# Performance work log

Measured on AMD Instinct MI355X. Metric: run time of the kernel, lower is better.

The kernel has to match this reference:

```python
import jax, jax.numpy as jnp
import numpy as np

B, C, D, H, W = 2, 64, 8, 32, 32  # identity f/g mappings => intermediate_channels == input_channels == 64


def setup_inputs() -> dict:
    key = jax.random.key(0)
    k1, k2 = jax.random.split(key)
    x = jax.random.normal(k1, (B, C, D, H, W), dtype=jnp.float32)
    # w_mapping: 1x1 conv, intermediate_channels -> input_channels (here 64 -> 64)
    w_weight = jax.random.normal(k2, (C, C), dtype=jnp.float32) * (1.0 / np.sqrt(C))
    w_bias = jnp.zeros((C,), dtype=jnp.float32)
    return {"x": x, "w_weight": w_weight, "w_bias": w_bias}


def reference(x, w_weight, w_bias):
    b, c = x.shape[0], x.shape[1]
    spatial = x.shape[2:]
    n = int(np.prod(spatial))
    # f/g mappings are identity -> q, k, v are all the flattened input
    x_flat = x.reshape(b, c, n)              # [B, C, N]
    q = jnp.transpose(x_flat, (0, 2, 1))     # [B, N, C] (f_mapping_i, permuted)
    k = x_flat                               # [B, C, N] (f_mapping_j)
    v = jnp.transpose(x_flat, (0, 2, 1))     # [B, N, C] (g_x, permuted)
    f = jnp.einsum('bic,bcj->bij', q, k)     # [B, N, N] dot-product similarity
    f_norm = jax.nn.softmax(f, axis=-1)
    y = jnp.einsum('bij,bjc->bic', f_norm, v)  # [B, N, C]
    y = jnp.transpose(y, (0, 2, 1)).reshape(b, c, *spatial)  # [B, C, D, H, W]
    # w_mapping: 1x1 conv (pointwise linear over channels) + bias
    w_y = jnp.einsum('bc...,oc->bo...', y, w_weight) + w_bias.reshape((1, c) + (1,) * len(spatial))
    z = w_y + x  # residual
    return z
```

## Files before the change

### kernel.cpp

```cpp
#include <hip/hip_runtime.h>
#include <hip/hip_bf16.h>


constexpr int NC = 64;
constexpr int NN = 8192;
constexpr int NKV = 128;

typedef __attribute__((ext_vector_type(8))) short bf16x8;
typedef __attribute__((ext_vector_type(4))) float f32x4;

static __device__ __forceinline__ short f2bf(float f) {
    union { float f; unsigned u; } v; v.f = f;
    unsigned r = v.u + 0x7FFFu + ((v.u >> 16) & 1u);
    return (short)(r >> 16);
}
static __device__ __forceinline__ float bf2f(short h) {
    union { unsigned u; float f; } v;
    v.u = ((unsigned)(unsigned short)h) << 16;
    return v.f;
}

__global__ __launch_bounds__(256) void prep_kernel(
    const float* __restrict__ x, short* __restrict__ Xjc, short* __restrict__ Xcj)
{
    __shared__ short T[64 * 64];
    const int tid = threadIdx.x;
    const int jt = blockIdx.x;
    const int b  = blockIdx.y;
    const int bo = b * NC * NN;
    const int sc = tid >> 2, sq = tid & 3;

    const float* xr = x + bo + sc * NN + jt * 64 + sq * 16;
    float fl[16];
    *(float4*)&fl[0]  = *(const float4*)(xr + 0);
    *(float4*)&fl[4]  = *(const float4*)(xr + 4);
    *(float4*)&fl[8]  = *(const float4*)(xr + 8);
    *(float4*)&fl[12] = *(const float4*)(xr + 12);
    short h[16];
    #pragma unroll
    for (int e = 0; e < 16; ++e) h[e] = f2bf(fl[e]);

    bf16x8 v0, v1;
    #pragma unroll
    for (int e = 0; e < 8; ++e) { v0[e] = h[e]; v1[e] = h[8 + e]; }
    *(bf16x8*)&Xcj[bo + sc * NN + jt * 64 + sq * 16]     = v0;
    *(bf16x8*)&Xcj[bo + sc * NN + jt * 64 + sq * 16 + 8] = v1;

    #pragma unroll
    for (int jj = 0; jj < 16; ++jj) {
        int j = sq * 16 + jj;
        T[(j * 64 + sc) ^ ((j & 7) << 3)] = h[jj];
    }
    __syncthreads();

    const int jr = tid >> 2, cq = tid & 3;
    bf16x8 a0 = *(const bf16x8*)&T[(jr * 64 + cq * 16) ^ ((jr & 7) << 3)];
    bf16x8 a1 = *(const bf16x8*)&T[(jr * 64 + cq * 16 + 8) ^ ((jr & 7) << 3)];
    *(bf16x8*)&Xjc[bo + (jt * 64 + jr) * 64 + cq * 16]     = a0;
    *(bf16x8*)&Xjc[bo + (jt * 64 + jr) * 64 + cq * 16 + 8] = a1;
}

__global__ __launch_bounds__(256) void attn_fd_kernel(
    const short* __restrict__ Xjc, const short* __restrict__ Xcj,
    float* __restrict__ ypart, float* __restrict__ lpart, int tps)
{
    __shared__ short Pl[4][32 * 64];

    const int tid  = threadIdx.x;
    const int lane = tid & 63;
    const int wv   = tid >> 6;
    const int lo   = lane & 15;
    const int hi   = lane >> 4;

    const int b  = blockIdx.y;
    const int sp = blockIdx.z;
    const int bo = b * NC * NN;
    const int qbase = blockIdx.x * 128 + wv * 32;
    short* Pw = Pl[wv];

    bf16x8 qf[2][2];
    #pragma unroll
    for (int qs = 0; qs < 2; ++qs)
        #pragma unroll
        for (int kk = 0; kk < 2; ++kk)
            qf[qs][kk] = *(const bf16x8*)&Xjc[bo + (qbase + qs * 16 + lo) * 64 + kk * 32 + hi * 8];

    float mrow[2][4];
    #pragma unroll
    for (int qs = 0; qs < 2; ++qs) {
        float v = 0.0f;
        #pragma unroll
        for (int kk = 0; kk < 2; ++kk)
            #pragma unroll
            for (int e = 0; e < 8; ++e) { float q = bf2f(qf[qs][kk][e]); v += q * q; }
        v += __shfl_xor(v, 16);
        v += __shfl_xor(v, 32);
        #pragma unroll
        for (int r = 0; r < 4; ++r) mrow[qs][r] = __shfl(v, hi * 4 + r);
    }

    f32x4 acc[2][4];
    f32x4 lacc[2];
    #pragma unroll
    for (int qs = 0; qs < 2; ++qs) {
        #pragma unroll
        for (int ct = 0; ct < 4; ++ct)
            #pragma unroll
            for (int r = 0; r < 4; ++r) acc[qs][ct][r] = 0.0f;
        #pragma unroll
        for (int r = 0; r < 4; ++r) lacc[qs][r] = 0.0f;
    }
    bf16x8 ones;
    #pragma unroll
    for (int e = 0; e < 8; ++e) ones[e] = (short)0x3F80;

    const int jb0 = sp * tps, jb1 = jb0 + tps;
    bf16x8 kfc[4][2], kfn[4][2];
    #pragma unroll
    for (int jt = 0; jt < 4; ++jt)
        #pragma unroll
        for (int kk = 0; kk < 2; ++kk)
            kfc[jt][kk] = *(const bf16x8*)&Xjc[bo + (jb0 * 64 + jt * 16 + lo) * 64 + kk * 32 + hi * 8];

    for (int jb = jb0; jb < jb1; ++jb) {
        bf16x8 vf[4][2];
        #pragma unroll
        for (int ct = 0; ct < 4; ++ct)
            #pragma unroll
            for (int kk = 0; kk < 2; ++kk)
                vf[ct][kk] = *(const bf16x8*)&Xcj[bo + (ct * 16 + lo) * NN + jb * 64 + kk * 32 + hi * 8];
        const bool more = (jb + 1 < jb1);
        if (more) {
            #pragma unroll
            for (int jt = 0; jt < 4; ++jt)
                #pragma unroll
                for (int kk = 0; kk < 2; ++kk)
                    kfn[jt][kk] = *(const bf16x8*)&Xjc[bo + ((jb + 1) * 64 + jt * 16 + lo) * 64 + kk * 32 + hi * 8];
        }

        f32x4 s[2][4];
        #pragma unroll
        for (int qs = 0; qs < 2; ++qs)
            #pragma unroll
            for (int jt = 0; jt < 4; ++jt) {
                #pragma unroll
                for (int r = 0; r < 4; ++r) s[qs][jt][r] = 0.0f;
                #pragma unroll
                for (int kk = 0; kk < 2; ++kk)
                    s[qs][jt] = __builtin_amdgcn_mfma_f32_16x16x32_bf16(qf[qs][kk], kfc[jt][kk], s[qs][jt], 0, 0, 0);
            }

        #pragma unroll
        for (int qs = 0; qs < 2; ++qs)
            #pragma unroll
            for (int jt = 0; jt < 4; ++jt)
                #pragma unroll
                for (int r = 0; r < 4; ++r) {
                    float p = __expf(s[qs][jt][r] - mrow[qs][r]);
                    int i = qs * 16 + hi * 4 + r;
                    Pw[(i * 64 + jt * 16 + lo) ^ ((i & 7) << 3)] = f2bf(p);
                }
        asm volatile("s_waitcnt lgkmcnt(0)" ::: "memory");
        __builtin_amdgcn_sched_barrier(0);

        bf16x8 pf[2][2];
        #pragma unroll
        for (int qs = 0; qs < 2; ++qs)
            #pragma unroll
            for (int kk = 0; kk < 2; ++kk) {
                int row = qs * 16 + lo;
                pf[qs][kk] = *(const bf16x8*)&Pw[(row * 64 + kk * 32 + hi * 8) ^ ((row & 7) << 3)];
            }

        #pragma unroll
        for (int qs = 0; qs < 2; ++qs)
            #pragma unroll
            for (int kk = 0; kk < 2; ++kk)
                lacc[qs] = __builtin_amdgcn_mfma_f32_16x16x32_bf16(ones, pf[qs][kk], lacc[qs], 0, 0, 0);

        #pragma unroll
        for (int qs = 0; qs < 2; ++qs)
            #pragma unroll
            for (int ct = 0; ct < 4; ++ct)
                #pragma unroll
                for (int kk = 0; kk < 2; ++kk)
                    acc[qs][ct] = __builtin_amdgcn_mfma_f32_16x16x32_bf16(vf[ct][kk], pf[qs][kk], acc[qs][ct], 0, 0, 0);

        if (more) {
            #pragma unroll
            for (int jt = 0; jt < 4; ++jt)
                #pragma unroll
                for (int kk = 0; kk < 2; ++kk)
                    kfc[jt][kk] = kfn[jt][kk];
        }
    }

    float* yp = ypart + (size_t)(sp * 2 + b) * NC * NN;
    #pragma unroll
    for (int qs = 0; qs < 2; ++qs)
        #pragma unroll
        for (int ct = 0; ct < 4; ++ct)
            #pragma unroll
            for (int r = 0; r < 4; ++r) {
                int c = ct * 16 + hi * 4 + r;
                yp[c * NN + qbase + qs * 16 + lo] = acc[qs][ct][r];
            }
    if (hi == 0) {
        #pragma unroll
        for (int qs = 0; qs < 2; ++qs)
            lpart[(sp * 2 + b) * NN + qbase + qs * 16 + lo] = lacc[qs][0];
    }
}

__global__ __launch_bounds__(256) void combine_kernel(
    const float* __restrict__ x, const float* __restrict__ wmat,
    const float* __restrict__ wbias, const float* __restrict__ ypart,
    const float* __restrict__ lpart, float* __restrict__ out, int nsplit)
{
    const int tid  = threadIdx.x;
    const int lane = tid & 63;
    const int wv   = tid >> 6;
    const int lo   = lane & 15;
    const int hi   = lane >> 4;

    const int batch = blockIdx.y;
    const int b_off = batch * NC * NN;
    const int qwave = blockIdx.x * 64 + wv * 16;
    const int i     = qwave + lo;

    float L = 0.0f;
    for (int s = 0; s < nsplit; ++s) L += lpart[(s * 2 + batch) * NN + i];
    const float linv = 1.0f / L;

    float accm[4][4];
    #pragma unroll
    for (int ct = 0; ct < 4; ++ct)
        #pragma unroll
        for (int r = 0; r < 4; ++r) accm[ct][r] = 0.0f;
    for (int s = 0; s < nsplit; ++s) {
        const float* yp = ypart + (size_t)(s * 2 + batch) * NC * NN;
        #pragma unroll
        for (int ct = 0; ct < 4; ++ct)
            #pragma unroll
            for (int r = 0; r < 4; ++r) {
                int c = ct * 16 + hi * 4 + r;
                accm[ct][r] += yp[c * NN + qwave + lo];
            }
    }

    bf16x8 yf[2];
    #pragma unroll
    for (int kk = 0; kk < 2; ++kk)
        #pragma unroll
        for (int e = 0; e < 8; ++e)
            yf[kk][e] = f2bf(accm[kk * 2 + (e >> 2)][e & 3] * linv);

    f32x4 z[4];
    #pragma unroll
    for (int ot = 0; ot < 4; ++ot) {
        #pragma unroll
        for (int r = 0; r < 4; ++r) z[ot][r] = 0.0f;
        int o = ot * 16 + lo;
        #pragma unroll
        for (int kk = 0; kk < 2; ++kk) {
            float4 wa = *(const float4*)&wmat[o * 64 + kk * 32 + hi * 4];
            float4 wb = *(const float4*)&wmat[o * 64 + kk * 32 + 16 + hi * 4];
            bf16x8 wf;
            wf[0] = f2bf(wa.x); wf[1] = f2bf(wa.y); wf[2] = f2bf(wa.z); wf[3] = f2bf(wa.w);
            wf[4] = f2bf(wb.x); wf[5] = f2bf(wb.y); wf[6] = f2bf(wb.z); wf[7] = f2bf(wb.w);
            z[ot] = __builtin_amdgcn_mfma_f32_16x16x32_bf16(wf, yf[kk], z[ot], 0, 0, 0);
        }
    }

    #pragma unroll
    for (int ot = 0; ot < 4; ++ot)
        #pragma unroll
        for (int r = 0; r < 4; ++r) {
            int o = ot * 16 + hi * 4 + r;
            int idx = b_off + o * NN + qwave + lo;
            out[idx] = z[ot][r] + wbias[o] + x[idx];
        }
}

__global__ __launch_bounds__(256) void attn_nl_kernel(
    const float* __restrict__ x, const float* __restrict__ wmat,
    const float* __restrict__ wbias, float* __restrict__ out)
{
    __shared__ short Xcj[64 * 64];
    __shared__ short Xjc[64 * 64];
    __shared__ short Plds[4][16 * 64];

    const int tid  = threadIdx.x;
    const int lane = tid & 63;
    const int wv   = tid >> 6;
    const int lo   = lane & 15;
    const int hi   = lane >> 4;

    const int batch = blockIdx.y;
    const int b_off = batch * NC * NN;
    const int qwave = blockIdx.x * 64 + wv * 16;
    const int qrow  = qwave + lo;

    bf16x8 qf[2];
    #pragma unroll
    for (int kk = 0; kk < 2; ++kk)
        #pragma unroll
        for (int e = 0; e < 8; ++e) {
            int c = kk * 32 + hi * 8 + e;
            qf[kk][e] = f2bf(x[b_off + c * NN + qrow]);
        }

    f32x4 acc[4];
    #pragma unroll
    for (int ct = 0; ct < 4; ++ct)
        #pragma unroll
        for (int r = 0; r < 4; ++r) acc[ct][r] = 0.0f;
    float mrow[4], lrow[4];
    #pragma unroll
    for (int r = 0; r < 4; ++r) { mrow[r] = -INFINITY; lrow[r] = 0.0f; }

    const int sc = tid >> 2;
    const int sq = tid & 3;
    const float* xrow = x + b_off + sc * NN + sq * 16;

    for (int jb = 0; jb < NKV; ++jb) {
        const int jbase = jb * 64;
        __syncthreads();

        float fl[16];
        *(float4*)&fl[0]  = *(const float4*)(xrow + jbase + 0);
        *(float4*)&fl[4]  = *(const float4*)(xrow + jbase + 4);
        *(float4*)&fl[8]  = *(const float4*)(xrow + jbase + 8);
        *(float4*)&fl[12] = *(const float4*)(xrow + jbase + 12);
        short h[16];
        #pragma unroll
        for (int e = 0; e < 16; ++e) h[e] = f2bf(fl[e]);

        {
            bf16x8 v0, v1;
            #pragma unroll
            for (int e = 0; e < 8; ++e) { v0[e] = h[e]; v1[e] = h[8 + e]; }
            int base = sc * 64 + sq * 16;
            int sw = (sc & 7) << 3;
            *(bf16x8*)&Xcj[(base) ^ sw]     = v0;
            *(bf16x8*)&Xcj[(base + 8) ^ sw] = v1;
        }
        #pragma unroll
        for (int jj = 0; jj < 16; ++jj) {
            int j = sq * 16 + jj;
            Xjc[(j * 64 + sc) ^ ((j & 7) << 3)] = h[jj];
        }
        __syncthreads();

        f32x4 s[4];
        #pragma unroll
        for (int jt = 0; jt < 4; ++jt) {
            #pragma unroll
            for (int r = 0; r < 4; ++r) s[jt][r] = 0.0f;
            int j = jt * 16 + lo;
            #pragma unroll
            for (int kk = 0; kk < 2; ++kk) {
                bf16x8 kf = *(const bf16x8*)&Xjc[(j * 64 + kk * 32 + hi * 8) ^ ((j & 7) << 3)];
                s[jt] = __builtin_amdgcn_mfma_f32_16x16x32_bf16(qf[kk], kf, s[jt], 0, 0, 0);
            }
        }

        float tm[4];
        #pragma unroll
        for (int r = 0; r < 4; ++r)
            tm[r] = fmaxf(fmaxf(s[0][r], s[1][r]), fmaxf(s[2][r], s[3][r]));
        #pragma unroll
        for (int d = 1; d < 16; d <<= 1)
            #pragma unroll
            for (int r = 0; r < 4; ++r)
                tm[r] = fmaxf(tm[r], __shfl_xor(tm[r], d));

        float scl4[4];
        #pragma unroll
        for (int r = 0; r < 4; ++r) {
            float mnew = fmaxf(mrow[r], tm[r]);
            scl4[r] = __expf(mrow[r] - mnew);
            mrow[r] = mnew;
        }

        float rs[4] = {0.f, 0.f, 0.f, 0.f};
        #pragma unroll
        for (int jt = 0; jt < 4; ++jt)
            #pragma unroll
            for (int r = 0; r < 4; ++r) {
                float p = __expf(s[jt][r] - mrow[r]);
                rs[r] += p;
                int i = hi * 4 + r;
                Plds[wv][(i * 64 + jt * 16 + lo) ^ ((i & 7) << 3)] = f2bf(p);
            }
        #pragma unroll
        for (int d = 1; d < 16; d <<= 1)
            #pragma unroll
            for (int r = 0; r < 4; ++r)
                rs[r] += __shfl_xor(rs[r], d);
        #pragma unroll
        for (int r = 0; r < 4; ++r)
            lrow[r] = lrow[r] * scl4[r] + rs[r];

        {
            int srcl = (lo >> 2) << 4;
            float b0 = __shfl(scl4[0], srcl), b1 = __shfl(scl4[1], srcl);
            float b2 = __shfl(scl4[2], srcl), b3 = __shfl(scl4[3], srcl);
            int rr = lo & 3;
            float scl = rr == 0 ? b0 : rr == 1 ? b1 : rr == 2 ? b2 : b3;
            #pragma unroll
            for (int ct = 0; ct < 4; ++ct)
                #pragma unroll
                for (int r = 0; r < 4; ++r) acc[ct][r] *= scl;
        }

        asm volatile("s_waitcnt lgkmcnt(0)" ::: "memory");

        bf16x8 pf[2];
        #pragma unroll
        for (int kk = 0; kk < 2; ++kk)
            pf[kk] = *(const bf16x8*)&Plds[wv][(lo * 64 + kk * 32 + hi * 8) ^ ((lo & 7) << 3)];
        #pragma unroll
        for (int ct = 0; ct < 4; ++ct) {
            int c = ct * 16 + lo;
            #pragma unroll
            for (int kk = 0; kk < 2; ++kk) {
                bf16x8 vf = *(const bf16x8*)&Xcj[(c * 64 + kk * 32 + hi * 8) ^ ((c & 7) << 3)];
                acc[ct] = __builtin_amdgcn_mfma_f32_16x16x32_bf16(vf, pf[kk], acc[ct], 0, 0, 0);
            }
        }
    }

    float linv;
    {
        int srcl = (lo >> 2) << 4;
        float c0 = __shfl(lrow[0], srcl), c1 = __shfl(lrow[1], srcl);
        float c2 = __shfl(lrow[2], srcl), c3 = __shfl(lrow[3], srcl);
        int rr = lo & 3;
        float li = rr == 0 ? c0 : rr == 1 ? c1 : rr == 2 ? c2 : c3;
        linv = 1.0f / li;
    }

    bf16x8 yf[2];
    #pragma unroll
    for (int kk = 0; kk < 2; ++kk)
        #pragma unroll
        for (int e = 0; e < 8; ++e)
            yf[kk][e] = f2bf(acc[kk * 2 + (e >> 2)][e & 3] * linv);

    f32x4 z[4];
    #pragma unroll
    for (int ot = 0; ot < 4; ++ot) {
        #pragma unroll
        for (int r = 0; r < 4; ++r) z[ot][r] = 0.0f;
        int o = ot * 16 + lo;
        #pragma unroll
        for (int kk = 0; kk < 2; ++kk) {
            float4 wa = *(const float4*)&wmat[o * 64 + kk * 32 + hi * 4];
            float4 wb = *(const float4*)&wmat[o * 64 + kk * 32 + 16 + hi * 4];
            bf16x8 wf;
            wf[0] = f2bf(wa.x); wf[1] = f2bf(wa.y); wf[2] = f2bf(wa.z); wf[3] = f2bf(wa.w);
            wf[4] = f2bf(wb.x); wf[5] = f2bf(wb.y); wf[6] = f2bf(wb.z); wf[7] = f2bf(wb.w);
            z[ot] = __builtin_amdgcn_mfma_f32_16x16x32_bf16(wf, yf[kk], z[ot], 0, 0, 0);
        }
    }

    #pragma unroll
    for (int ot = 0; ot < 4; ++ot)
        #pragma unroll
        for (int r = 0; r < 4; ++r) {
            int o = ot * 16 + hi * 4 + r;
            int idx = b_off + o * NN + qwave + lo;
            out[idx] = z[ot][r] + wbias[o] + x[idx];
        }
}

extern "C" void kernel_launch(void* const* d_in, const int* in_sizes, int n_in,
                              void* d_out, int out_size, void* d_ws, size_t ws_size,
                              hipStream_t stream) {
    const float* x  = (const float*)d_in[0];
    const float* w  = (const float*)d_in[1];
    const float* b  = (const float*)d_in[2];
    float* out = (float*)d_out;

    const size_t xhalf = (size_t)2 * NC * NN;
    auto need = [&](int ns) -> size_t {
        return xhalf * 2 * sizeof(short)
             + (size_t)ns * 2 * NC * NN * sizeof(float)
             + (size_t)ns * 2 * NN * sizeof(float);
    };

    int ns = 0;
    if      (ws_size >= need(8)) ns = 8;
    else if (ws_size >= need(4)) ns = 4;
    else if (ws_size >= need(2)) ns = 2;
    else if (ws_size >= need(1)) ns = 1;

    if (ns) {
        short* Xjc = (short*)d_ws;
        short* Xcj = Xjc + xhalf;
        float* ypart = (float*)(Xcj + xhalf);
        float* lpart = ypart + (size_t)ns * 2 * NC * NN;
        const int tps = NKV / ns;
        prep_kernel<<<dim3(NKV, 2), 256, 0, stream>>>(x, Xjc, Xcj);
        attn_fd_kernel<<<dim3(NN / 128, 2, ns), 256, 0, stream>>>(Xjc, Xcj, ypart, lpart, tps);
        combine_kernel<<<dim3(NN / 64, 2), 256, 0, stream>>>(x, w, b, ypart, lpart, out, ns);
    } else {
        attn_nl_kernel<<<dim3(NN / 64, 2), 256, 0, stream>>>(x, w, b, out);
    }
}
```

Measured before the change: 195.7 us.

## Software-pipeline attention loop: overlap QK^T and exp of next tile with PV of previous

Restructures the flash-decoding inner loop into a prologue, a steady state and an epilogue. Each iteration computes S for tile t and writes its exp into one of two double-buffered LDS P buffers, while the PV and row-sum MFMAs consume the P of tile t-1 from the other buffer. The aim is to hide the exp/LDS write latency and the lgkm wait behind MFMA work and to drop the kfn register copy. In exchange it doubles per-wave LDS for P and may raise register pressure, since S, vf and pf are live together.

```diff
diff --git a/kernel.cpp b/kernel.cpp
--- a/kernel.cpp
+++ b/kernel.cpp
@@ -64,7 +64,7 @@
     const short* __restrict__ Xjc, const short* __restrict__ Xcj,
     float* __restrict__ ypart, float* __restrict__ lpart, int tps)
 {
-    __shared__ short Pl[4][32 * 64];
+    __shared__ short Pl[4][2][32 * 64];
 
     const int tid  = threadIdx.x;
     const int lane = tid & 63;
@@ -76,7 +76,7 @@
     const int sp = blockIdx.z;
     const int bo = b * NC * NN;
     const int qbase = blockIdx.x * 128 + wv * 32;
-    short* Pw = Pl[wv];
+    short* Pbuf[2] = { Pl[wv][0], Pl[wv][1] };
 
     bf16x8 qf[2][2];
     #pragma unroll
@@ -115,29 +115,15 @@
     for (int e = 0; e < 8; ++e) ones[e] = (short)0x3F80;
 
     const int jb0 = sp * tps, jb1 = jb0 + tps;
-    bf16x8 kfc[4][2], kfn[4][2];
+
+    bf16x8 kfc[4][2];
     #pragma unroll
     for (int jt = 0; jt < 4; ++jt)
         #pragma unroll
         for (int kk = 0; kk < 2; ++kk)
             kfc[jt][kk] = *(const bf16x8*)&Xjc[bo + (jb0 * 64 + jt * 16 + lo) * 64 + kk * 32 + hi * 8];
 
-    for (int jb = jb0; jb < jb1; ++jb) {
-        bf16x8 vf[4][2];
-        #pragma unroll
-        for (int ct = 0; ct < 4; ++ct)
-            #pragma unroll
-            for (int kk = 0; kk < 2; ++kk)
-                vf[ct][kk] = *(const bf16x8*)&Xcj[bo + (ct * 16 + lo) * NN + jb * 64 + kk * 32 + hi * 8];
-        const bool more = (jb + 1 < jb1);
-        if (more) {
-            #pragma unroll
-            for (int jt = 0; jt < 4; ++jt)
-                #pragma unroll
-                for (int kk = 0; kk < 2; ++kk)
-                    kfn[jt][kk] = *(const bf16x8*)&Xjc[bo + ((jb + 1) * 64 + jt * 16 + lo) * 64 + kk * 32 + hi * 8];
-        }
-
+    {
         f32x4 s[2][4];
         #pragma unroll
         for (int qs = 0; qs < 2; ++qs)
@@ -149,7 +135,13 @@
                 for (int kk = 0; kk < 2; ++kk)
                     s[qs][jt] = __builtin_amdgcn_mfma_f32_16x16x32_bf16(qf[qs][kk], kfc[jt][kk], s[qs][jt], 0, 0, 0);
             }
-
+        if (jb0 + 1 < jb1) {
+            #pragma unroll
+            for (int jt = 0; jt < 4; ++jt)
+                #pragma unroll
+                for (int kk = 0; kk < 2; ++kk)
+                    kfc[jt][kk] = *(const bf16x8*)&Xjc[bo + ((jb0 + 1) * 64 + jt * 16 + lo) * 64 + kk * 32 + hi * 8];
+        }
         #pragma unroll
         for (int qs = 0; qs < 2; ++qs)
             #pragma unroll
@@ -158,8 +150,39 @@
                 for (int r = 0; r < 4; ++r) {
                     float p = __expf(s[qs][jt][r] - mrow[qs][r]);
                     int i = qs * 16 + hi * 4 + r;
-                    Pw[(i * 64 + jt * 16 + lo) ^ ((i & 7) << 3)] = f2bf(p);
+                    Pbuf[0][(i * 64 + jt * 16 + lo) ^ ((i & 7) << 3)] = f2bf(p);
                 }
+    }
+
+    for (int t = jb0 + 1; t < jb1; ++t) {
+        const int pw = (t - jb0) & 1;
+        bf16x8 vf[4][2];
+        #pragma unroll
+        for (int ct = 0; ct < 4; ++ct)
+            #pragma unroll
+            for (int kk = 0; kk < 2; ++kk)
+                vf[ct][kk] = *(const bf16x8*)&Xcj[bo + (ct * 16 + lo) * NN + (t - 1) * 64 + kk * 32 + hi * 8];
+
+        f32x4 s[2][4];
+        #pragma unroll
+        for (int qs = 0; qs < 2; ++qs)
+            #pragma unroll
+            for (int jt = 0; jt < 4; ++jt) {
+                #pragma unroll
+                for (int r = 0; r < 4; ++r) s[qs][jt][r] = 0.0f;
+                #pragma unroll
+                for (int kk = 0; kk < 2; ++kk)
+                    s[qs][jt] = __builtin_amdgcn_mfma_f32_16x16x32_bf16(qf[qs][kk], kfc[jt][kk], s[qs][jt], 0, 0, 0);
+            }
+
+        if (t + 1 < jb1) {
+            #pragma unroll
+            for (int jt = 0; jt < 4; ++jt)
+                #pragma unroll
+                for (int kk = 0; kk < 2; ++kk)
+                    kfc[jt][kk] = *(const bf16x8*)&Xjc[bo + ((t + 1) * 64 + jt * 16 + lo) * 64 + kk * 32 + hi * 8];
+        }
+
         asm volatile("s_waitcnt lgkmcnt(0)" ::: "memory");
         __builtin_amdgcn_sched_barrier(0);
 
@@ -169,7 +192,7 @@
             #pragma unroll
             for (int kk = 0; kk < 2; ++kk) {
                 int row = qs * 16 + lo;
-                pf[qs][kk] = *(const bf16x8*)&Pw[(row * 64 + kk * 32 + hi * 8) ^ ((row & 7) << 3)];
+                pf[qs][kk] = *(const bf16x8*)&Pbuf[pw ^ 1][(row * 64 + kk * 32 + hi * 8) ^ ((row & 7) << 3)];
             }
 
         #pragma unroll
@@ -177,7 +200,6 @@
             #pragma unroll
             for (int kk = 0; kk < 2; ++kk)
                 lacc[qs] = __builtin_amdgcn_mfma_f32_16x16x32_bf16(ones, pf[qs][kk], lacc[qs], 0, 0, 0);
-
         #pragma unroll
         for (int qs = 0; qs < 2; ++qs)
             #pragma unroll
@@ -186,13 +208,50 @@
                 for (int kk = 0; kk < 2; ++kk)
                     acc[qs][ct] = __builtin_amdgcn_mfma_f32_16x16x32_bf16(vf[ct][kk], pf[qs][kk], acc[qs][ct], 0, 0, 0);
 
-        if (more) {
+        #pragma unroll
+        for (int qs = 0; qs < 2; ++qs)
             #pragma unroll
             for (int jt = 0; jt < 4; ++jt)
                 #pragma unroll
+                for (int r = 0; r < 4; ++r) {
+                    float p = __expf(s[qs][jt][r] - mrow[qs][r]);
+                    int i = qs * 16 + hi * 4 + r;
+                    Pbuf[pw][(i * 64 + jt * 16 + lo) ^ ((i & 7) << 3)] = f2bf(p);
+                }
+    }
+
+    {
+        const int lastp = (jb1 - 1 - jb0) & 1;
+        bf16x8 vf[4][2];
+        #pragma unroll
+        for (int ct = 0; ct < 4; ++ct)
+            #pragma unroll
+            for (int kk = 0; kk < 2; ++kk)
+                vf[ct][kk] = *(const bf16x8*)&Xcj[bo + (ct * 16 + lo) * NN + (jb1 - 1) * 64 + kk * 32 + hi * 8];
+
+        asm volatile("s_waitcnt lgkmcnt(0)" ::: "memory");
+        __builtin_amdgcn_sched_barrier(0);
+
+        bf16x8 pf[2][2];
+        #pragma unroll
+        for (int qs = 0; qs < 2; ++qs)
+            #pragma unroll
+            for (int kk = 0; kk < 2; ++kk) {
+                int row = qs * 16 + lo;
+                pf[qs][kk] = *(const bf16x8*)&Pbuf[lastp][(row * 64 + kk * 32 + hi * 8) ^ ((row & 7) << 3)];
+            }
+        #pragma unroll
+        for (int qs = 0; qs < 2; ++qs)
+            #pragma unroll
+            for (int kk = 0; kk < 2; ++kk)
+                lacc[qs] = __builtin_amdgcn_mfma_f32_16x16x32_bf16(ones, pf[qs][kk], lacc[qs], 0, 0, 0);
+        #pragma unroll
+        for (int qs = 0; qs < 2; ++qs)
+            #pragma unroll
+            for (int ct = 0; ct < 4; ++ct)
+                #pragma unroll
                 for (int kk = 0; kk < 2; ++kk)
-                    kfc[jt][kk] = kfn[jt][kk];
-        }
+                    acc[qs][ct] = __builtin_amdgcn_mfma_f32_16x16x32_bf16(vf[ct][kk], pf[qs][kk], acc[qs][ct], 0, 0, 0);
     }
 
     float* yp = ypart + (size_t)(sp * 2 + b) * NC * NN;
```

Result: slower. 212.8 us (+8.7%).
